# Kernel optimization log

Measured on AMD Instinct MI355X. Metric: run time of the kernel, lower is better.

Reference implementation:

```python
import jax, jax.numpy as jnp
import numpy as np

B, J = 131072, 24
# SMPL skeleton parent indices (root = joint 0)
SMPL_PARENTS = np.array([-1, 0, 0, 0, 1, 2, 3, 4, 5, 6, 7, 8, 9, 9, 9, 12, 13, 14, 16, 17, 18, 19, 20, 21], dtype=np.int64)


def setup_inputs() -> dict:
    key = jax.random.key(0)
    k1, k2 = jax.random.split(key)
    positions = jax.random.normal(k1, (B, J, 3), dtype=jnp.float32)
    rotations = jax.random.normal(k2, (B, J, 4), dtype=jnp.float32)
    return {"parents": SMPL_PARENTS, "positions": positions, "rotations": rotations}


def _quat_to_rotmat(q):
    # q: [B, J, 4] (w, x, y, z); normalize then standard unit-quaternion rotation matrix
    q = q / jnp.linalg.norm(q, axis=-1, keepdims=True)
    qw, qx, qy, qz = q[..., 0], q[..., 1], q[..., 2], q[..., 3]
    x2, y2, z2 = qx + qx, qy + qy, qz + qz
    xx, yy, zz = qx * x2, qy * y2, qz * z2
    xy, yz, xz = qx * y2, qy * z2, qx * z2
    wx, wy, wz = qw * x2, qw * y2, qw * z2
    row0 = jnp.stack([1.0 - (yy + zz), xy - wz, xz + wy], axis=-1)
    row1 = jnp.stack([xy + wz, 1.0 - (xx + zz), yz - wx], axis=-1)
    row2 = jnp.stack([xz - wy, yz + wx, 1.0 - (xx + yy)], axis=-1)
    return jnp.stack([row0, row1, row2], axis=-2)  # [B, J, 3, 3]


def _local_transforms(positions, rotations):
    R = _quat_to_rotmat(rotations)                       # [B, J, 3, 3]
    top = jnp.concatenate([R, positions[..., None]], axis=-1)  # [B, J, 3, 4]
    bottom = jnp.broadcast_to(
        jnp.array([0.0, 0.0, 0.0, 1.0], dtype=rotations.dtype), top.shape[:2] + (1, 4))
    return jnp.concatenate([top, bottom], axis=-2)       # [B, J, 4, 4]


def reference(parents, positions, rotations):
    parents = np.asarray(parents)  # static skeleton topology
    locals_ = _local_transforms(positions, rotations)    # [B, J, 4, 4]
    n_joints = parents.shape[0]
    # Sequential parent-child chain over the (small, static) joint tree.
    g = [locals_[:, 0]]
    for jt in range(1, n_joints):
        g.append(jnp.matmul(g[int(parents[jt])], locals_[:, jt]))
    globals_ = jnp.stack(g, axis=1)                      # [B, J, 4, 4]
    p = globals_[:, :, :, 3]                             # homogeneous positions [B, J, 4]
    return p[:, :, :3] / p[:, :, 3:4]                    # [B, J, 3]
```

## Files before the change

### kernel.cpp

```cpp
#include <hip/hip_runtime.h>


typedef float f32x4 __attribute__((ext_vector_type(4)));

struct M { float r0,r1,r2,r3,r4,r5,r6,r7,r8,tx,ty,tz; };

__device__ __forceinline__ M loc(float a, float b, float c, float d,
                                 float px, float py, float pz) {
    float inv = rsqrtf(a*a + b*b + c*c + d*d);
    float qw = a*inv, qx = b*inv, qy = c*inv, qz = d*inv;
    float x2 = qx+qx, y2 = qy+qy, z2 = qz+qz;
    float xx = qx*x2, yy = qy*y2, zz = qz*z2;
    float xy = qx*y2, yz = qy*z2, xz = qx*z2;
    float wx = qw*x2, wy = qw*y2, wz = qw*z2;
    M m;
    m.r0 = 1.f-(yy+zz); m.r1 = xy-wz;       m.r2 = xz+wy;
    m.r3 = xy+wz;       m.r4 = 1.f-(xx+zz); m.r5 = yz-wx;
    m.r6 = xz-wy;       m.r7 = yz+wx;       m.r8 = 1.f-(xx+yy);
    m.tx = px; m.ty = py; m.tz = pz;
    return m;
}

__device__ __forceinline__ M mul(const M& a, const M& b) {
    M c;
    c.r0 = a.r0*b.r0 + a.r1*b.r3 + a.r2*b.r6;
    c.r1 = a.r0*b.r1 + a.r1*b.r4 + a.r2*b.r7;
    c.r2 = a.r0*b.r2 + a.r1*b.r5 + a.r2*b.r8;
    c.r3 = a.r3*b.r0 + a.r4*b.r3 + a.r5*b.r6;
    c.r4 = a.r3*b.r1 + a.r4*b.r4 + a.r5*b.r7;
    c.r5 = a.r3*b.r2 + a.r4*b.r5 + a.r5*b.r8;
    c.r6 = a.r6*b.r0 + a.r7*b.r3 + a.r8*b.r6;
    c.r7 = a.r6*b.r1 + a.r7*b.r4 + a.r8*b.r7;
    c.r8 = a.r6*b.r2 + a.r7*b.r5 + a.r8*b.r8;
    c.tx = a.r0*b.tx + a.r1*b.ty + a.r2*b.tz + a.tx;
    c.ty = a.r3*b.tx + a.r4*b.ty + a.r5*b.tz + a.ty;
    c.tz = a.r6*b.tx + a.r7*b.ty + a.r8*b.tz + a.tz;
    return c;
}

#define SPB    48
#define NTHR   256
#define RPITCH 97
#define PPITCH 73

constexpr int MT0[6]  = {0,1,2,4,7,10};
constexpr int PR0[6]  = {-1,0,0,1,3,4};
constexpr int MT1[8]  = {0,2,5,8,11,3,6,9};
constexpr int PR1[8]  = {-1,0,1,2,3,0,5,6};
constexpr int MT2[11] = {0,3,6,9,12,15,13,16,18,20,22};
constexpr int PR2[11] = {-1,0,1,2,3,4,3,6,7,8,9};
constexpr int MT3[9]  = {0,3,6,9,14,17,19,21,23};
constexpr int PR3[9]  = {-1,0,1,2,3,4,5,6,7};

template<int NM>
__device__ __forceinline__ void read_pos(const int (&MT)[NM],
                                         const float* __restrict__ P,
                                         float* __restrict__ pb) {
#pragma unroll
    for (int k = 0; k < NM; ++k) {
        pb[3*k+0] = P[3*MT[k]+0];
        pb[3*k+1] = P[3*MT[k]+1];
        pb[3*k+2] = P[3*MT[k]+2];
    }
}

template<int NM>
__device__ __forceinline__ void run_chain(const int (&MT)[NM], const int (&PR)[NM],
                                          int WS,
                                          const float* __restrict__ R,
                                          const float* __restrict__ pb,
                                          float* __restrict__ O) {
    M G[NM];
    G[0] = loc(R[0], R[1], R[2], R[3], pb[0], pb[1], pb[2]);
    if (WS == 0) { O[0]=G[0].tx; O[1]=G[0].ty; O[2]=G[0].tz; }
#pragma unroll
    for (int k = 1; k < NM; ++k) {
        const int j = MT[k];
        M L = loc(R[4*j], R[4*j+1], R[4*j+2], R[4*j+3],
                  pb[3*k], pb[3*k+1], pb[3*k+2]);
        G[k] = mul(G[PR[k]], L);
        if (k >= WS) { O[3*j]=G[k].tx; O[3*j+1]=G[k].ty; O[3*j+2]=G[k].tz; }
    }
}

__global__ __launch_bounds__(NTHR, 3) void fk_kernel(
    const float* __restrict__ rot,
    const float* __restrict__ pos,
    float*       __restrict__ out,
    int B)
{
    __shared__ float ldsR[SPB * RPITCH];
    __shared__ float ldsP[SPB * PPITCH];

    const int t = threadIdx.x;
    const size_t baseR = (size_t)blockIdx.x * (SPB*96);
    const size_t baseP = (size_t)blockIdx.x * (SPB*72);
    const size_t limR  = (size_t)B * 96;
    const size_t limP  = (size_t)B * 72;

    f32x4 vr[5], vp[4];
#pragma unroll
    for (int i = 0; i < 5; ++i) {
        const bool c = (i < 4) || (t < 128);
        const size_t gi = baseR + (size_t)(i*1024 + 4*t);
        f32x4 v = {0.f,0.f,0.f,0.f};
        if (c && gi < limR) v = *(const f32x4*)(rot + gi);
        vr[i] = v;
    }
#pragma unroll
    for (int i = 0; i < 4; ++i) {
        const bool c = (i < 3) || (t < 96);
        const size_t gi = baseP + (size_t)(i*1024 + 4*t);
        f32x4 v = {0.f,0.f,0.f,0.f};
        if (c && gi < limP) v = *(const f32x4*)(pos + gi);
        vp[i] = v;
    }
#pragma unroll
    for (int i = 0; i < 5; ++i) {
        if ((i < 4) || (t < 128)) {
            const int f = i*1024 + 4*t;
            const int s = f / 96, r = f - 96*s;
            float* d = ldsR + s*RPITCH + r;
            d[0]=vr[i].x; d[1]=vr[i].y; d[2]=vr[i].z; d[3]=vr[i].w;
        }
    }
#pragma unroll
    for (int i = 0; i < 4; ++i) {
        if ((i < 3) || (t < 96)) {
            const int f = i*1024 + 4*t;
            const int s = f / 72, r = f - 72*s;
            float* d = ldsP + s*PPITCH + r;
            d[0]=vp[i].x; d[1]=vp[i].y; d[2]=vp[i].z; d[3]=vp[i].w;
        }
    }
    __syncthreads();

    const int w = t >> 6, l = t & 63;
    const int b = blockIdx.x * SPB + l;
    const bool act = (l < SPB) && (b < B);
    const float* R = ldsR + l * RPITCH;
    const float* P = ldsP + l * PPITCH;
    float*       O = ldsP + l * PPITCH;

    float pb[33];
    if (act) {
        switch (w) {
            case 0:  read_pos(MT0, P, pb); break;
            case 1:  read_pos(MT1, P, pb); break;
            case 2:  read_pos(MT2, P, pb); break;
            default: read_pos(MT3, P, pb); break;
        }
    }
    __syncthreads();

    if (act) {
        switch (w) {
            case 0:  run_chain(MT0, PR0, 0, R, pb, O); break;
            case 1:  run_chain(MT1, PR1, 2, R, pb, O); break;
            case 2:  run_chain(MT2, PR2, 4, R, pb, O); break;
            default: run_chain(MT3, PR3, 4, R, pb, O); break;
        }
    }
    __syncthreads();

#pragma unroll
    for (int n = 0; n < 4; ++n) {
        if ((n < 3) || (t < 96)) {
            const int F = n*1024 + 4*t;
            const int s = F / 72, r = F - 72*s;
            const size_t gi = baseP + (size_t)F;
            if (gi < limP) {
                f32x4 v = { ldsP[s*PPITCH+r+0], ldsP[s*PPITCH+r+1],
                            ldsP[s*PPITCH+r+2], ldsP[s*PPITCH+r+3] };
                *(f32x4*)(out + gi) = v;
            }
        }
    }
}

extern "C" void kernel_launch(void* const* d_in, const int* in_sizes, int n_in,
                              void* d_out, int out_size, void* d_ws, size_t ws_size,
                              hipStream_t stream) {
    const int B = out_size / 72;
    const void* rot = nullptr;
    const void* pos = nullptr;
    for (int i = 0; i < n_in; ++i) {
        if      (in_sizes[i] == B * 96) rot = d_in[i];
        else if (in_sizes[i] == B * 72) pos = d_in[i];
    }
    if (!rot) rot = d_in[2];
    if (!pos) pos = d_in[1];

    const int grid = (B + SPB - 1) / SPB;
    fk_kernel<<<grid, NTHR, 0, stream>>>(
        (const float*)rot, (const float*)pos, (float*)d_out, B);
}
```

Baseline: 130.0 us.

## Use persistent grid with register prefetch of next chunk overlapping compute

Switches to a persistent kernel with a fixed grid of 768 blocks. Each block loops over chunks of 48 samples and prefetches the next chunk's rotations and positions into registers while computing the current one, aiming to hide global-load latency behind the FK chain math. A separate LDS output buffer replaces in-place reuse of the position buffer, and rotations are read as aligned 16-byte vectors with a padded pitch of 100. In exchange it uses more LDS per block and more live registers, and it adds an extra barrier per iteration.

```diff
diff --git a/kernel.cpp b/kernel.cpp
--- a/kernel.cpp
+++ b/kernel.cpp
@@ -40,8 +40,10 @@
 
 #define SPB    48
 #define NTHR   256
-#define RPITCH 97
+#define GRID   768
+#define RPITCH 100
 #define PPITCH 73
+#define OPITCH 73
 
 constexpr int MT0[6]  = {0,1,2,4,7,10};
 constexpr int PR0[6]  = {-1,0,0,1,3,4};
@@ -53,31 +55,22 @@
 constexpr int PR3[9]  = {-1,0,1,2,3,4,5,6,7};
 
 template<int NM>
-__device__ __forceinline__ void read_pos(const int (&MT)[NM],
-                                         const float* __restrict__ P,
-                                         float* __restrict__ pb) {
-#pragma unroll
-    for (int k = 0; k < NM; ++k) {
-        pb[3*k+0] = P[3*MT[k]+0];
-        pb[3*k+1] = P[3*MT[k]+1];
-        pb[3*k+2] = P[3*MT[k]+2];
-    }
-}
-
-template<int NM>
 __device__ __forceinline__ void run_chain(const int (&MT)[NM], const int (&PR)[NM],
                                           int WS,
                                           const float* __restrict__ R,
-                                          const float* __restrict__ pb,
+                                          const float* __restrict__ P,
                                           float* __restrict__ O) {
     M G[NM];
-    G[0] = loc(R[0], R[1], R[2], R[3], pb[0], pb[1], pb[2]);
+    {
+        f32x4 q = *(const f32x4*)(R);
+        G[0] = loc(q.x, q.y, q.z, q.w, P[0], P[1], P[2]);
+    }
     if (WS == 0) { O[0]=G[0].tx; O[1]=G[0].ty; O[2]=G[0].tz; }
 #pragma unroll
     for (int k = 1; k < NM; ++k) {
         const int j = MT[k];
-        M L = loc(R[4*j], R[4*j+1], R[4*j+2], R[4*j+3],
-                  pb[3*k], pb[3*k+1], pb[3*k+2]);
+        f32x4 q = *(const f32x4*)(R + 4*j);
+        M L = loc(q.x, q.y, q.z, q.w, P[3*j], P[3*j+1], P[3*j+2]);
         G[k] = mul(G[PR[k]], L);
         if (k >= WS) { O[3*j]=G[k].tx; O[3*j+1]=G[k].ty; O[3*j+2]=G[k].tz; }
     }
@@ -89,90 +82,112 @@
     float*       __restrict__ out,
     int B)
 {
-    __shared__ float ldsR[SPB * RPITCH];
+    __shared__ __align__(16) float ldsR[SPB * RPITCH];
     __shared__ float ldsP[SPB * PPITCH];
+    __shared__ float ldsO[SPB * OPITCH];
 
     const int t = threadIdx.x;
-    const size_t baseR = (size_t)blockIdx.x * (SPB*96);
-    const size_t baseP = (size_t)blockIdx.x * (SPB*72);
-    const size_t limR  = (size_t)B * 96;
-    const size_t limP  = (size_t)B * 72;
+    const int nch = (B + SPB - 1) / SPB;
+    const size_t limR = (size_t)B * 96;
+    const size_t limP = (size_t)B * 72;
+
+    const int w = t >> 6, l = t & 63;
 
     f32x4 vr[5], vp[4];
-#pragma unroll
-    for (int i = 0; i < 5; ++i) {
-        const bool c = (i < 4) || (t < 128);
-        const size_t gi = baseR + (size_t)(i*1024 + 4*t);
-        f32x4 v = {0.f,0.f,0.f,0.f};
-        if (c && gi < limR) v = *(const f32x4*)(rot + gi);
-        vr[i] = v;
-    }
-#pragma unroll
-    for (int i = 0; i < 4; ++i) {
-        const bool c = (i < 3) || (t < 96);
-        const size_t gi = baseP + (size_t)(i*1024 + 4*t);
-        f32x4 v = {0.f,0.f,0.f,0.f};
-        if (c && gi < limP) v = *(const f32x4*)(pos + gi);
-        vp[i] = v;
-    }
-#pragma unroll
-    for (int i = 0; i < 5; ++i) {
-        if ((i < 4) || (t < 128)) {
-            const int f = i*1024 + 4*t;
-            const int s = f / 96, r = f - 96*s;
-            float* d = ldsR + s*RPITCH + r;
-            d[0]=vr[i].x; d[1]=vr[i].y; d[2]=vr[i].z; d[3]=vr[i].w;
-        }
-    }
-#pragma unroll
-    for (int i = 0; i < 4; ++i) {
-        if ((i < 3) || (t < 96)) {
-            const int f = i*1024 + 4*t;
-            const int s = f / 72, r = f - 72*s;
-            float* d = ldsP + s*PPITCH + r;
-            d[0]=vp[i].x; d[1]=vp[i].y; d[2]=vp[i].z; d[3]=vp[i].w;
-        }
-    }
-    __syncthreads();
-
-    const int w = t >> 6, l = t & 63;
-    const int b = blockIdx.x * SPB + l;
-    const bool act = (l < SPB) && (b < B);
-    const float* R = ldsR + l * RPITCH;
-    const float* P = ldsP + l * PPITCH;
-    float*       O = ldsP + l * PPITCH;
-
-    float pb[33];
-    if (act) {
-        switch (w) {
-            case 0:  read_pos(MT0, P, pb); break;
-            case 1:  read_pos(MT1, P, pb); break;
-            case 2:  read_pos(MT2, P, pb); break;
-            default: read_pos(MT3, P, pb); break;
-        }
-    }
-    __syncthreads();
-
-    if (act) {
-        switch (w) {
-            case 0:  run_chain(MT0, PR0, 0, R, pb, O); break;
-            case 1:  run_chain(MT1, PR1, 2, R, pb, O); break;
-            case 2:  run_chain(MT2, PR2, 4, R, pb, O); break;
-            default: run_chain(MT3, PR3, 4, R, pb, O); break;
-        }
-    }
-    __syncthreads();
-
-#pragma unroll
-    for (int n = 0; n < 4; ++n) {
-        if ((n < 3) || (t < 96)) {
-            const int F = n*1024 + 4*t;
-            const int s = F / 72, r = F - 72*s;
-            const size_t gi = baseP + (size_t)F;
-            if (gi < limP) {
-                f32x4 v = { ldsP[s*PPITCH+r+0], ldsP[s*PPITCH+r+1],
-                            ldsP[s*PPITCH+r+2], ldsP[s*PPITCH+r+3] };
-                *(f32x4*)(out + gi) = v;
+
+    int c = blockIdx.x;
+    {
+        const size_t baseR = (size_t)c * (SPB*96);
+        const size_t baseP = (size_t)c * (SPB*72);
+#pragma unroll
+        for (int i = 0; i < 5; ++i) {
+            const bool g = (i < 4) || (t < 128);
+            const size_t gi = baseR + (size_t)(i*1024 + 4*t);
+            f32x4 v = {0.f,0.f,0.f,0.f};
+            if (g && gi < limR) v = *(const f32x4*)(rot + gi);
+            vr[i] = v;
+        }
+#pragma unroll
+        for (int i = 0; i < 4; ++i) {
+            const bool g = (i < 3) || (t < 96);
+            const size_t gi = baseP + (size_t)(i*1024 + 4*t);
+            f32x4 v = {0.f,0.f,0.f,0.f};
+            if (g && gi < limP) v = *(const f32x4*)(pos + gi);
+            vp[i] = v;
+        }
+    }
+
+    for (; c < nch; c += GRID) {
+        __syncthreads();
+
+#pragma unroll
+        for (int i = 0; i < 5; ++i) {
+            if ((i < 4) || (t < 128)) {
+                const int f = i*1024 + 4*t;
+                const int s = f / 96, r = f - 96*s;
+                float* d = ldsR + s*RPITCH + r;
+                d[0]=vr[i].x; d[1]=vr[i].y; d[2]=vr[i].z; d[3]=vr[i].w;
+            }
+        }
+#pragma unroll
+        for (int i = 0; i < 4; ++i) {
+            if ((i < 3) || (t < 96)) {
+                const int f = i*1024 + 4*t;
+                const int s = f / 72, r = f - 72*s;
+                float* d = ldsP + s*PPITCH + r;
+                d[0]=vp[i].x; d[1]=vp[i].y; d[2]=vp[i].z; d[3]=vp[i].w;
+            }
+        }
+        __syncthreads();
+
+        const int cn = c + GRID;
+        if (cn < nch) {
+            const size_t baseR = (size_t)cn * (SPB*96);
+            const size_t baseP = (size_t)cn * (SPB*72);
+#pragma unroll
+            for (int i = 0; i < 5; ++i) {
+                const bool g = (i < 4) || (t < 128);
+                const size_t gi = baseR + (size_t)(i*1024 + 4*t);
+                f32x4 v = {0.f,0.f,0.f,0.f};
+                if (g && gi < limR) v = *(const f32x4*)(rot + gi);
+                vr[i] = v;
+            }
+#pragma unroll
+            for (int i = 0; i < 4; ++i) {
+                const bool g = (i < 3) || (t < 96);
+                const size_t gi = baseP + (size_t)(i*1024 + 4*t);
+                f32x4 v = {0.f,0.f,0.f,0.f};
+                if (g && gi < limP) v = *(const f32x4*)(pos + gi);
+                vp[i] = v;
+            }
+        }
+
+        const int b = c * SPB + l;
+        if ((l < SPB) && (b < B)) {
+            const float* R = ldsR + l * RPITCH;
+            const float* P = ldsP + l * PPITCH;
+            float*       O = ldsO + l * OPITCH;
+            switch (w) {
+                case 0:  run_chain(MT0, PR0, 0, R, P, O); break;
+                case 1:  run_chain(MT1, PR1, 2, R, P, O); break;
+                case 2:  run_chain(MT2, PR2, 4, R, P, O); break;
+                default: run_chain(MT3, PR3, 4, R, P, O); break;
+            }
+        }
+        __syncthreads();
+
+        const size_t baseP = (size_t)c * (SPB*72);
+#pragma unroll
+        for (int n = 0; n < 4; ++n) {
+            if ((n < 3) || (t < 96)) {
+                const int F = n*1024 + 4*t;
+                const int s = F / 72, r = F - 72*s;
+                const size_t gi = baseP + (size_t)F;
+                if (gi < limP) {
+                    f32x4 v = { ldsO[s*OPITCH+r+0], ldsO[s*OPITCH+r+1],
+                                ldsO[s*OPITCH+r+2], ldsO[s*OPITCH+r+3] };
+                    *(f32x4*)(out + gi) = v;
+                }
             }
         }
     }
@@ -191,7 +206,8 @@
     if (!rot) rot = d_in[2];
     if (!pos) pos = d_in[1];
 
-    const int grid = (B + SPB - 1) / SPB;
+    const int nch  = (B + SPB - 1) / SPB;
+    const int grid = (nch < GRID) ? nch : GRID;
     fk_kernel<<<grid, NTHR, 0, stream>>>(
         (const float*)rot, (const float*)pos, (float*)d_out, B);
 }
```

Measured after the change: 142.2 us. 9.4% more time.
